# Kernel tuning notes

Measured on AMD Instinct MI355X. Metric: run time of the kernel, lower is better.

## Reference

```python
import jax, jax.numpy as jnp
import numpy as np

N_NODES = 50000


def _gcn_layer(h_in, W, b, src, dst, dis):
    # GCNConv: h = x @ W; out[i] = sum_{j->i} (dis[j]*dis[i]) h[j] + dis[i]^2 h[i] + b
    h = h_in @ W                               # [N, out]
    coef = dis[src] * dis[dst]                 # [E]
    agg = jax.ops.segment_sum(h[src] * coef[:, None], dst, num_segments=N_NODES)
    agg = agg + h * (dis * dis)[:, None]       # self-loop term
    return agg + b


def setup_inputs() -> dict:
    key = jax.random.key(0)
    ks = jax.random.split(key, 8)
    F_in, H, C = 256, 128, 16
    E = 800000
    x = jax.random.normal(ks[0], (N_NODES, F_in), dtype=jnp.float32)
    edge_index = jax.random.randint(ks[1], (2, E), 0, N_NODES, dtype=jnp.int64)
    s = lambda fan_in: 1.0 / np.sqrt(fan_in)
    W1 = jax.random.normal(ks[2], (F_in, H), dtype=jnp.float32) * s(F_in)
    b1 = jnp.zeros((H,), jnp.float32)
    W2 = jax.random.normal(ks[3], (H, H // 2), dtype=jnp.float32) * s(H)
    b2 = jnp.zeros((H // 2,), jnp.float32)
    W3 = jax.random.normal(ks[4], (H // 2, C), dtype=jnp.float32) * s(H // 2)
    b3 = jnp.zeros((C,), jnp.float32)
    return {"x": x, "edge_index": edge_index, "W1": W1, "b1": b1,
            "W2": W2, "b2": b2, "W3": W3, "b3": b3}


def reference(x, edge_index, W1, b1, W2, b2, W3, b3):
    src, dst = edge_index[0], edge_index[1]
    # degree with self-loops: deg[i] = 1 + in-degree(i)
    deg = jnp.ones((N_NODES,), x.dtype).at[dst].add(1.0)
    dis = jax.lax.rsqrt(deg)
    h = _gcn_layer(x, W1, b1, src, dst, dis)
    h = jax.nn.relu(h)
    h = _gcn_layer(h, W2, b2, src, dst, dis)
    h = jax.nn.relu(h)
    return _gcn_layer(h, W3, b3, src, dst, dis)
```

## Files before the change

### kernel.cpp

```cpp
#include <hip/hip_runtime.h>

#define N_NODES 50000
#define CAP 64

typedef _Float16 h4v __attribute__((ext_vector_type(4)));
typedef _Float16 h8v __attribute__((ext_vector_type(8)));
typedef float    f4v __attribute__((ext_vector_type(4)));

template <int K, int N>
__device__ inline void pack_one(const float* __restrict__ W, _Float16* __restrict__ Wp,
                                int idx) {
    const int KB = K / 32, NB_ = N / 16;
    if (idx >= NB_ * KB * 64) return;
    int lane = idx & 63;
    int fb   = idx >> 6;
    int kb   = fb % KB, nb = fb / KB;
    int lm = lane & 15, g = lane >> 4;
    h8v v;
    #pragma unroll
    for (int j = 0; j < 8; ++j) {
        int k = kb * 32 + g * 4 + (j & 3) + ((j >> 2) << 4);
        v[j] = (_Float16)W[(size_t)k * N + nb * 16 + lm];
    }
    *(h8v*)&Wp[(size_t)idx * 8] = v;
}

__global__ __launch_bounds__(256) void k_prep(const unsigned* __restrict__ ei,
                                              unsigned* __restrict__ flag,
                                              int* __restrict__ cnt, int NB,
                                              const float* __restrict__ W1,
                                              const float* __restrict__ W2,
                                              const float* __restrict__ W3,
                                              _Float16* __restrict__ Wp1,
                                              _Float16* __restrict__ Wp2,
                                              _Float16* __restrict__ Wp3) {
    const int bid = blockIdx.x, tid = threadIdx.x;
    if (bid < NB) {
        int i = bid * 256 + tid;
        if (i < N_NODES) cnt[i] = 0;
        return;
    }
    if (bid == NB) {
        __shared__ unsigned nz;
        if (tid == 0) nz = 0u;
        __syncthreads();
        unsigned v = 0u;
        for (int i = tid; i < 1024; i += 256) v |= ei[2 * i + 1];
        if (v) atomicOr(&nz, 1u);
        __syncthreads();
        if (tid == 0) flag[0] = (nz == 0u) ? 1u : 0u;
        return;
    }
    int pb = bid - NB - 1;
    if (pb < 16)      pack_one<256, 128>(W1, Wp1, pb * 256 + tid);
    else if (pb < 20) pack_one<128, 64>(W2, Wp2, (pb - 16) * 256 + tid);
    else              pack_one<64, 16>(W3, Wp3, (pb - 20) * 256 + tid);
}

__global__ __launch_bounds__(256) void k_mega1(const int* __restrict__ ei,
                                               const unsigned* __restrict__ flag,
                                               int E, int GB1,
                                               int* __restrict__ cnt,
                                               int* __restrict__ recs,
                                               const float* __restrict__ x,
                                               const _Float16* __restrict__ Wp1,
                                               _Float16* __restrict__ h16) {
    const int tid = threadIdx.x;
    const int bid = blockIdx.x;
    const int gcand = bid / 5;
    const bool is_gemm = (bid % 5 == 0) && (gcand < GB1);
    if (!is_gemm) {
        int fidx = bid - min((bid + 4) / 5, GB1);
        int e = fidx * 256 + tid;
        if (e < E) {
            int fl = flag[0];
            int s = fl ? ei[2 * e] : ei[e];
            int d = fl ? ei[2 * (E + e)] : ei[E + e];
            int slot = atomicAdd(&cnt[d], 1);
            if (slot < CAP) recs[d * CAP + slot] = s;
        }
        return;
    }
    const int K = 256, N = 128, BM = 64, BK = 32, PAD = 4, KB = K / 32;
    const int NF = N / 16;
    __shared__ _Float16 at[BM][BK + PAD];

    const int w    = tid >> 6;
    const int lane = tid & 63;
    const int g    = lane >> 4;
    const int lm   = lane & 15;
    const int bm0  = gcand * BM;

    f4v acc[NF];
    #pragma unroll
    for (int n = 0; n < NF; ++n) acc[n] = (f4v){0.f, 0.f, 0.f, 0.f};

    for (int kb = 0; kb < KB; ++kb) {
        int k0 = kb * 32;
        for (int idx = tid; idx < BM * (BK / 4); idx += 256) {
            int row = idx >> 3;
            int q   = idx & 7;
            int r   = bm0 + row;
            float4 v = make_float4(0.f, 0.f, 0.f, 0.f);
            if (r < N_NODES) v = *(const float4*)&x[(size_t)r * K + k0 + q * 4];
            h4v hv = {(_Float16)v.x, (_Float16)v.y, (_Float16)v.z, (_Float16)v.w};
            *(h4v*)&at[row][q * 4] = hv;
        }
        __syncthreads();

        int m = 16 * w + lm;
        h4v alo = *(const h4v*)&at[m][g * 4];
        h4v ahi = *(const h4v*)&at[m][16 + g * 4];
        h8v a = {alo[0], alo[1], alo[2], alo[3], ahi[0], ahi[1], ahi[2], ahi[3]};

        #pragma unroll
        for (int n = 0; n < NF; ++n) {
            h8v b = *(const h8v*)&Wp1[(size_t)((n * KB + kb) * 64 + lane) * 8];
            acc[n] = __builtin_amdgcn_mfma_f32_16x16x32_f16(a, b, acc[n], 0, 0, 0);
        }
        __syncthreads();
    }

    #pragma unroll
    for (int r = 0; r < 4; ++r) {
        int row = bm0 + 16 * w + 4 * g + r;
        if (row < N_NODES) {
            #pragma unroll
            for (int n = 0; n < NF; ++n)
                h16[(size_t)row * N + n * 16 + lm] = (_Float16)acc[n][r];
        }
    }
}

template <int F, int N>
__global__ __launch_bounds__(256) void k_gather_gemm(const int* __restrict__ recs,
                                                     const int* __restrict__ cnt,
                                                     const _Float16* __restrict__ hin,
                                                     const float* __restrict__ bias,
                                                     const _Float16* __restrict__ Wp,
                                                     _Float16* __restrict__ hout) {
    const int PAD = 8, KB = F / 32, NF = N / 16;
    __shared__ _Float16 at[64][F + PAD];
    const int tid = threadIdx.x;
    const int bm0 = blockIdx.x * 64;

    const int QP = F / 8;
    for (int s = tid; s < 64 * QP; s += 256) {
        int row = s / QP;
        int q   = s % QP;
        int d   = bm0 + row;
        h8v o = {};
        if (d < N_NODES) {
            int deg = cnt[d];
            int beg = d * CAP, end = beg + min(deg, CAP);
            float fd = 1.0f + (float)deg;
            float acc[8] = {};
            int i = beg;
            for (; i + 4 <= end; i += 4) {
                int s0 = recs[i], s1 = recs[i + 1], s2 = recs[i + 2], s3 = recs[i + 3];
                float c0 = rsqrtf(fd * (1.0f + (float)cnt[s0]));
                float c1 = rsqrtf(fd * (1.0f + (float)cnt[s1]));
                float c2 = rsqrtf(fd * (1.0f + (float)cnt[s2]));
                float c3 = rsqrtf(fd * (1.0f + (float)cnt[s3]));
                h8v v0 = *(const h8v*)&hin[(size_t)s0 * F + q * 8];
                h8v v1 = *(const h8v*)&hin[(size_t)s1 * F + q * 8];
                h8v v2 = *(const h8v*)&hin[(size_t)s2 * F + q * 8];
                h8v v3 = *(const h8v*)&hin[(size_t)s3 * F + q * 8];
                #pragma unroll
                for (int j = 0; j < 8; ++j) {
                    acc[j] = fmaf(c0, (float)v0[j], fmaf(c1, (float)v1[j], acc[j]));
                    acc[j] = fmaf(c2, (float)v2[j], fmaf(c3, (float)v3[j], acc[j]));
                }
            }
            for (; i < end; ++i) {
                int s0 = recs[i];
                float c0 = rsqrtf(fd * (1.0f + (float)cnt[s0]));
                h8v v0 = *(const h8v*)&hin[(size_t)s0 * F + q * 8];
                #pragma unroll
                for (int j = 0; j < 8; ++j)
                    acc[j] = fmaf(c0, (float)v0[j], acc[j]);
            }
            float invd = 1.0f / fd;
            h8v hd = *(const h8v*)&hin[(size_t)d * F + q * 8];
            #pragma unroll
            for (int j = 0; j < 8; ++j) {
                float t = fmaf((float)hd[j], invd, acc[j]) + bias[q * 8 + j];
                o[j] = (_Float16)fmaxf(t, 0.f);
            }
        }
        *(h8v*)&at[row][q * 8] = o;
    }
    __syncthreads();

    const int w    = tid >> 6;
    const int lane = tid & 63;
    const int g    = lane >> 4;
    const int lm   = lane & 15;

    f4v acc2[NF];
    #pragma unroll
    for (int n = 0; n < NF; ++n) acc2[n] = (f4v){0.f, 0.f, 0.f, 0.f};

    #pragma unroll
    for (int kb = 0; kb < KB; ++kb) {
        int k0 = kb * 32;
        int m = 16 * w + lm;
        h4v alo = *(const h4v*)&at[m][k0 + g * 4];
        h4v ahi = *(const h4v*)&at[m][k0 + 16 + g * 4];
        h8v a = {alo[0], alo[1], alo[2], alo[3], ahi[0], ahi[1], ahi[2], ahi[3]};
        #pragma unroll
        for (int n = 0; n < NF; ++n) {
            h8v b = *(const h8v*)&Wp[(size_t)((n * KB + kb) * 64 + lane) * 8];
            acc2[n] = __builtin_amdgcn_mfma_f32_16x16x32_f16(a, b, acc2[n], 0, 0, 0);
        }
    }

    #pragma unroll
    for (int r = 0; r < 4; ++r) {
        int row = bm0 + 16 * w + 4 * g + r;
        if (row < N_NODES) {
            #pragma unroll
            for (int n = 0; n < NF; ++n)
                hout[(size_t)row * N + n * 16 + lm] = (_Float16)acc2[n][r];
        }
    }
}

__global__ __launch_bounds__(256) void k_gather_final(const int* __restrict__ recs,
                                                      const int* __restrict__ cnt,
                                                      const _Float16* __restrict__ hin,
                                                      const float* __restrict__ bias,
                                                      float* __restrict__ out) {
    const int F = 16, QP = 2;
    int tid = blockIdx.x * blockDim.x + threadIdx.x;
    int d = tid / QP;
    int q = tid % QP;
    if (d >= N_NODES) return;
    int deg = cnt[d];
    int beg = d * CAP, end = beg + min(deg, CAP);
    float fd = 1.0f + (float)deg;
    float acc[8] = {};
    int i = beg;
    for (; i + 2 <= end; i += 2) {
        int s0 = recs[i], s1 = recs[i + 1];
        float c0 = rsqrtf(fd * (1.0f + (float)cnt[s0]));
        float c1 = rsqrtf(fd * (1.0f + (float)cnt[s1]));
        h8v v0 = *(const h8v*)&hin[(size_t)s0 * F + q * 8];
        h8v v1 = *(const h8v*)&hin[(size_t)s1 * F + q * 8];
        #pragma unroll
        for (int j = 0; j < 8; ++j)
            acc[j] = fmaf(c0, (float)v0[j], fmaf(c1, (float)v1[j], acc[j]));
    }
    if (i < end) {
        int s0 = recs[i];
        float c0 = rsqrtf(fd * (1.0f + (float)cnt[s0]));
        h8v v0 = *(const h8v*)&hin[(size_t)s0 * F + q * 8];
        #pragma unroll
        for (int j = 0; j < 8; ++j)
            acc[j] = fmaf(c0, (float)v0[j], acc[j]);
    }
    float invd = 1.0f / fd;
    h8v hd = *(const h8v*)&hin[(size_t)d * F + q * 8];
    #pragma unroll
    for (int j = 0; j < 8; ++j)
        acc[j] = fmaf((float)hd[j], invd, acc[j]) + bias[q * 8 + j];

    float* op = &out[(size_t)d * F + q * 8];
    *(float4*)op       = make_float4(acc[0], acc[1], acc[2], acc[3]);
    *(float4*)(op + 4) = make_float4(acc[4], acc[5], acc[6], acc[7]);
}

extern "C" void kernel_launch(void* const* d_in, const int* in_sizes, int n_in,
                              void* d_out, int out_size, void* d_ws, size_t ws_size,
                              hipStream_t stream) {
    const float* x  = (const float*)d_in[0];
    const int*   ei = (const int*)d_in[1];
    const float* W1 = (const float*)d_in[2];
    const float* b1 = (const float*)d_in[3];
    const float* W2 = (const float*)d_in[4];
    const float* b2 = (const float*)d_in[5];
    const float* W3 = (const float*)d_in[6];
    const float* b3 = (const float*)d_in[7];
    float* out = (float*)d_out;

    const int E  = in_sizes[1] / 2;
    const int NB = (N_NODES + 255) / 256;
    const int FB = (E + 255) / 256;
    const int GB = (N_NODES + 63) / 64;

    char* ws = (char*)d_ws;
    size_t off = 0;
    auto alloc = [&](size_t bytes) -> void* {
        void* p = ws + off;
        off += (bytes + 255) & ~(size_t)255;
        return p;
    };
    unsigned*  flag   = (unsigned*)alloc(256);
    int*       cnt    = (int*)alloc((size_t)N_NODES * sizeof(int));
    int*       recs   = (int*)alloc((size_t)N_NODES * CAP * sizeof(int));
    _Float16*  Wp1    = (_Float16*)alloc((size_t)8 * 8 * 64 * 8 * sizeof(_Float16));
    _Float16*  Wp2    = (_Float16*)alloc((size_t)4 * 4 * 64 * 8 * sizeof(_Float16));
    _Float16*  Wp3    = (_Float16*)alloc((size_t)1 * 2 * 64 * 8 * sizeof(_Float16));
    _Float16*  h16a   = (_Float16*)alloc((size_t)N_NODES * 128 * sizeof(_Float16));
    _Float16*  h16b   = (_Float16*)alloc((size_t)N_NODES * 64 * sizeof(_Float16));
    _Float16*  h16c   = (_Float16*)alloc((size_t)N_NODES * 16 * sizeof(_Float16));

    k_prep<<<NB + 1 + 16 + 4 + 1, 256, 0, stream>>>((const unsigned*)ei, flag, cnt, NB,
                                                    W1, W2, W3, Wp1, Wp2, Wp3);

    k_mega1<<<GB + FB, 256, 0, stream>>>(ei, flag, E, GB, cnt, recs, x, Wp1, h16a);

    k_gather_gemm<128, 64><<<GB, 256, 0, stream>>>(recs, cnt, h16a, b1, Wp2, h16b);
    k_gather_gemm<64, 16><<<GB, 256, 0, stream>>>(recs, cnt, h16b, b2, Wp3, h16c);
    k_gather_final<<<(N_NODES * 2 + 255) / 256, 256, 0, stream>>>(recs, cnt, h16c, b3, out);
}
```

Baseline: 140.2 us.

## Narrow CSR records to 16-bit and batch edge fills per thread

Source indices in the bucketed adjacency are now stored as unsigned short instead of int, which halves the record footprint that every gather kernel reads. The fill blocks each handle 8 edges per thread with batched loads and atomics. They are interleaved with the GEMM blocks using a ratio computed on the host, which cuts the number of fill blocks. The 16-bit storage only holds while the node count stays below 65536, and the fill blocks now do more serial work each.

```diff
diff --git a/kernel.cpp b/kernel.cpp
--- a/kernel.cpp
+++ b/kernel.cpp
@@ -2,6 +2,7 @@
 
 #define N_NODES 50000
 #define CAP 64
+#define EPT 8
 
 typedef _Float16 h4v __attribute__((ext_vector_type(4)));
 typedef _Float16 h8v __attribute__((ext_vector_type(8)));
@@ -59,28 +60,43 @@
 
 __global__ __launch_bounds__(256) void k_mega1(const int* __restrict__ ei,
                                                const unsigned* __restrict__ flag,
-                                               int E, int GB1,
+                                               int E, int GB1, int FBn, int m,
                                                int* __restrict__ cnt,
-                                               int* __restrict__ recs,
+                                               unsigned short* __restrict__ recs,
                                                const float* __restrict__ x,
                                                const _Float16* __restrict__ Wp1,
                                                _Float16* __restrict__ h16) {
     const int tid = threadIdx.x;
     const int bid = blockIdx.x;
-    const int gcand = bid / 5;
-    const bool is_gemm = (bid % 5 == 0) && (gcand < GB1);
-    if (!is_gemm) {
-        int fidx = bid - min((bid + 4) / 5, GB1);
-        int e = fidx * 256 + tid;
-        if (e < E) {
-            int fl = flag[0];
-            int s = fl ? ei[2 * e] : ei[e];
-            int d = fl ? ei[2 * (E + e)] : ei[E + e];
-            int slot = atomicAdd(&cnt[d], 1);
-            if (slot < CAP) recs[d * CAP + slot] = s;
-        }
+    const bool is_fill = (m >= 2) && (bid % m == 1) && (bid / m < FBn);
+    if (is_fill) {
+        int f = bid / m;
+        int base = f * (256 * EPT) + tid;
+        int fl = flag[0];
+        int s[EPT], d[EPT];
+        #pragma unroll
+        for (int k = 0; k < EPT; ++k) {
+            int e = base + k * 256;
+            if (e < E) {
+                s[k] = fl ? ei[2 * e] : ei[e];
+                d[k] = fl ? ei[2 * (E + e)] : ei[E + e];
+            } else {
+                s[k] = -1; d[k] = 0;
+            }
+        }
+        int slot[EPT];
+        #pragma unroll
+        for (int k = 0; k < EPT; ++k)
+            slot[k] = (s[k] >= 0) ? atomicAdd(&cnt[d[k]], 1) : CAP;
+        #pragma unroll
+        for (int k = 0; k < EPT; ++k)
+            if (slot[k] < CAP) recs[d[k] * CAP + slot[k]] = (unsigned short)s[k];
         return;
     }
+    int fb = (m >= 2) ? min((bid + m - 2) / m, FBn) : 0;
+    int gcand = bid - fb;
+    if (gcand >= GB1) return;
+
     const int K = 256, N = 128, BM = 64, BK = 32, PAD = 4, KB = K / 32;
     const int NF = N / 16;
     __shared__ _Float16 at[BM][BK + PAD];
@@ -108,9 +124,9 @@
         }
         __syncthreads();
 
-        int m = 16 * w + lm;
-        h4v alo = *(const h4v*)&at[m][g * 4];
-        h4v ahi = *(const h4v*)&at[m][16 + g * 4];
+        int mm = 16 * w + lm;
+        h4v alo = *(const h4v*)&at[mm][g * 4];
+        h4v ahi = *(const h4v*)&at[mm][16 + g * 4];
         h8v a = {alo[0], alo[1], alo[2], alo[3], ahi[0], ahi[1], ahi[2], ahi[3]};
 
         #pragma unroll
@@ -133,7 +149,7 @@
 }
 
 template <int F, int N>
-__global__ __launch_bounds__(256) void k_gather_gemm(const int* __restrict__ recs,
+__global__ __launch_bounds__(256) void k_gather_gemm(const unsigned short* __restrict__ recs,
                                                      const int* __restrict__ cnt,
                                                      const _Float16* __restrict__ hin,
                                                      const float* __restrict__ bias,
@@ -204,9 +220,9 @@
     #pragma unroll
     for (int kb = 0; kb < KB; ++kb) {
         int k0 = kb * 32;
-        int m = 16 * w + lm;
-        h4v alo = *(const h4v*)&at[m][k0 + g * 4];
-        h4v ahi = *(const h4v*)&at[m][k0 + 16 + g * 4];
+        int mm = 16 * w + lm;
+        h4v alo = *(const h4v*)&at[mm][k0 + g * 4];
+        h4v ahi = *(const h4v*)&at[mm][k0 + 16 + g * 4];
         h8v a = {alo[0], alo[1], alo[2], alo[3], ahi[0], ahi[1], ahi[2], ahi[3]};
         #pragma unroll
         for (int n = 0; n < NF; ++n) {
@@ -226,7 +242,7 @@
     }
 }
 
-__global__ __launch_bounds__(256) void k_gather_final(const int* __restrict__ recs,
+__global__ __launch_bounds__(256) void k_gather_final(const unsigned short* __restrict__ recs,
                                                       const int* __restrict__ cnt,
                                                       const _Float16* __restrict__ hin,
                                                       const float* __restrict__ bias,
@@ -283,10 +299,12 @@
     const float* b3 = (const float*)d_in[7];
     float* out = (float*)d_out;
 
-    const int E  = in_sizes[1] / 2;
-    const int NB = (N_NODES + 255) / 256;
-    const int FB = (E + 255) / 256;
-    const int GB = (N_NODES + 63) / 64;
+    const int E   = in_sizes[1] / 2;
+    const int NB  = (N_NODES + 255) / 256;
+    const int GB  = (N_NODES + 63) / 64;
+    const int FBn = (E + 256 * EPT - 1) / (256 * EPT);
+    const int total = GB + FBn;
+    const int m   = total / FBn;
 
     char* ws = (char*)d_ws;
     size_t off = 0;
@@ -295,20 +313,20 @@
         off += (bytes + 255) & ~(size_t)255;
         return p;
     };
-    unsigned*  flag   = (unsigned*)alloc(256);
-    int*       cnt    = (int*)alloc((size_t)N_NODES * sizeof(int));
-    int*       recs   = (int*)alloc((size_t)N_NODES * CAP * sizeof(int));
-    _Float16*  Wp1    = (_Float16*)alloc((size_t)8 * 8 * 64 * 8 * sizeof(_Float16));
-    _Float16*  Wp2    = (_Float16*)alloc((size_t)4 * 4 * 64 * 8 * sizeof(_Float16));
-    _Float16*  Wp3    = (_Float16*)alloc((size_t)1 * 2 * 64 * 8 * sizeof(_Float16));
-    _Float16*  h16a   = (_Float16*)alloc((size_t)N_NODES * 128 * sizeof(_Float16));
-    _Float16*  h16b   = (_Float16*)alloc((size_t)N_NODES * 64 * sizeof(_Float16));
-    _Float16*  h16c   = (_Float16*)alloc((size_t)N_NODES * 16 * sizeof(_Float16));
+    unsigned*       flag = (unsigned*)alloc(256);
+    int*            cnt  = (int*)alloc((size_t)N_NODES * sizeof(int));
+    unsigned short* recs = (unsigned short*)alloc((size_t)N_NODES * CAP * sizeof(unsigned short));
+    _Float16*       Wp1  = (_Float16*)alloc((size_t)8 * 8 * 64 * 8 * sizeof(_Float16));
+    _Float16*       Wp2  = (_Float16*)alloc((size_t)4 * 4 * 64 * 8 * sizeof(_Float16));
+    _Float16*       Wp3  = (_Float16*)alloc((size_t)1 * 2 * 64 * 8 * sizeof(_Float16));
+    _Float16*       h16a = (_Float16*)alloc((size_t)N_NODES * 128 * sizeof(_Float16));
+    _Float16*       h16b = (_Float16*)alloc((size_t)N_NODES * 64 * sizeof(_Float16));
+    _Float16*       h16c = (_Float16*)alloc((size_t)N_NODES * 16 * sizeof(_Float16));
 
     k_prep<<<NB + 1 + 16 + 4 + 1, 256, 0, stream>>>((const unsigned*)ei, flag, cnt, NB,
                                                     W1, W2, W3, Wp1, Wp2, Wp3);
 
-    k_mega1<<<GB + FB, 256, 0, stream>>>(ei, flag, E, GB, cnt, recs, x, Wp1, h16a);
+    k_mega1<<<total, 256, 0, stream>>>(ei, flag, E, GB, FBn, m, cnt, recs, x, Wp1, h16a);
 
     k_gather_gemm<128, 64><<<GB, 256, 0, stream>>>(recs, cnt, h16a, b1, Wp2, h16b);
     k_gather_gemm<64, 16><<<GB, 256, 0, stream>>>(recs, cnt, h16b, b2, Wp3, h16c);
```

Result: faster. 137.3 us (-2.0%).
